# Kernel optimization log

Hardware: AMD Instinct MI355X
Metric: run time of the kernel (lower is better)

## Reference

```python
import jax, jax.numpy as jnp
import numpy as np

W_DIM, B_DIM, S = 8, 8, 900  # patches: [W, B, 1, 30, 30] -> seq_len 900


def setup_inputs() -> dict:
    key = jax.random.key(0)
    ks = jax.random.split(key, 8)
    radar = jax.random.normal(ks[0], (W_DIM, B_DIM, 1, 30, 30), jnp.float32)
    dmde = jax.random.normal(ks[1], (W_DIM, B_DIM, 1, 30, 30), jnp.float32)
    gumbel_u = jax.random.uniform(ks[2], (B_DIM * W_DIM, S, S), jnp.float32)
    # MHA with embed_dim=1 -> all projections are scalars (xavier-ish init)
    Wq = jax.random.normal(ks[3], (), jnp.float32)
    Wk = jax.random.normal(ks[4], (), jnp.float32)
    Wv = jax.random.normal(ks[5], (), jnp.float32)
    Wo = jax.random.normal(ks[6], (), jnp.float32)
    bq = jnp.zeros((), jnp.float32)
    bk = jnp.zeros((), jnp.float32)
    bv = jnp.zeros((), jnp.float32)
    bo = jnp.zeros((), jnp.float32)
    ln_gamma = jnp.ones((), jnp.float32)
    ln_beta = jnp.zeros((), jnp.float32)
    attn_residual_scale = jnp.asarray(1e-9, jnp.float32)
    return dict(radar_patches=radar, dmde_out_patches=dmde, gumbel_u=gumbel_u,
                Wq=Wq, bq=bq, Wk=Wk, bk=bk, Wv=Wv, bv=bv, Wo=Wo, bo=bo,
                ln_gamma=ln_gamma, ln_beta=ln_beta,
                attn_residual_scale=attn_residual_scale)


def reference(radar_patches, dmde_out_patches, gumbel_u, Wq, bq, Wk, bk, Wv, bv,
              Wo, bo, ln_gamma, ln_beta, attn_residual_scale):
    Wd, B = radar_patches.shape[0], radar_patches.shape[1]
    # [W,B,1,30,30] -> [B*W, S]
    radar = jnp.transpose(radar_patches, (1, 0, 2, 3, 4)).reshape(B * Wd, -1)
    mde = jnp.transpose(dmde_out_patches, (1, 0, 2, 3, 4)).reshape(B * Wd, -1)
    # --- cross attention, embed_dim = head_dim = 1 (scale = 1/sqrt(1) = 1) ---
    q = radar * Wq + bq
    k = mde * Wk + bk
    v = mde * Wv + bv
    attn = jax.nn.softmax(jnp.einsum('ni,nj->nij', q, k), axis=-1)  # [N,S,S]
    attended = jnp.einsum('nij,nj->ni', attn, v) * Wo + bo           # [N,S]
    # LayerNorm over last dim of size 1 (degenerate: output == ln_beta)
    x = (radar + attended)[..., None]                                # [N,S,1]
    mu = jnp.mean(x, axis=-1, keepdims=True)
    var = jnp.mean((x - mu) ** 2, axis=-1, keepdims=True)
    attended_out = (x - mu) / jnp.sqrt(var + 1e-5) * ln_gamma + ln_beta
    # --- hard gumbel attention gather/scatter, fully mask-vectorized ---
    valid = (radar != 0).astype(radar.dtype)                          # [N,S]
    noise = -jnp.log(-jnp.log(gumbel_u + 1e-8) + 1e-8)
    p = jax.nn.softmax(attn + noise, axis=-1)  # temperature = 1.0
    idx = jnp.argmax(p, axis=-1)                                      # [N,S]
    y_hard = jax.nn.one_hot(idx, p.shape[-1], dtype=p.dtype)
    y = jax.lax.stop_gradient(y_hard - p) + p                         # straight-through
    src = radar * valid   # invalid rows contribute nothing (matches per-row loop)
    out_seq = jnp.einsum('nts,nt->ns', y, src)[..., None]             # [N,S,1]
    combined = valid[..., None] * (out_seq != 0).astype(out_seq.dtype)
    out_seq = out_seq + combined * (attn_residual_scale * attended_out)
    # [N,S] -> [B,W,S] -> [B,1,S,W]
    out = out_seq[..., 0].reshape(B, Wd, -1).transpose(0, 2, 1)[:, None]
    return out
```

## Files before the change

### kernel.cpp

```cpp
#include <hip/hip_runtime.h>
#include <cfloat>

#define SS 900
#define WD 8
#define BD 8
#define NROWS 64
#define OUT_ELEMS (BD * SS * WD)
#define NQ 225
#define ROWS_PER_BLK 16
#define BLKS_PER_N 57
#define CAP 128

__global__ __launch_bounds__(256) void rel_zero(float4* __restrict__ out4) {
    int i = blockIdx.x * 256 + threadIdx.x;
    if (i < OUT_ELEMS / 4) out4[i] = make_float4(0.f, 0.f, 0.f, 0.f);
}

__global__ __launch_bounds__(256) void rel_main(
    const float* __restrict__ radar,
    const float* __restrict__ mde,
    const float* __restrict__ gumbel,
    const float* __restrict__ pWq, const float* __restrict__ pbq,
    const float* __restrict__ pWk, const float* __restrict__ pbk,
    float* __restrict__ out)
{
    const int tid   = threadIdx.x;
    const int n     = blockIdx.x / BLKS_PER_N;
    const int tbase = (blockIdx.x - n * BLKS_PER_N) * ROWS_PER_BLK;
    const int b     = n >> 3;
    const int w     = n & 7;

    __shared__ float4 ks4[NQ + 1];
    __shared__ float  s_red[8];
    __shared__ float  s_q[ROWS_PER_BLK], s_m[ROWS_PER_BLK], s_D[ROWS_PER_BLK];
    __shared__ unsigned long long s_win[ROWS_PER_BLK];
    __shared__ int    s_cnt;
    __shared__ int    s_qs[CAP];
    __shared__ float  s_qu[CAP];

    if (tid == 0) s_cnt = 0;
    if (tid < ROWS_PER_BLK) s_win[tid] = 0ULL;

    const float wk = pWk[0], bk0 = pbk[0];
    float kmin = FLT_MAX, kmax = -FLT_MAX;
    if (tid < NQ) {
        const float4* __restrict__ m4p = (const float4*)(mde + (size_t)(w * BD + b) * SS);
        float4 mq = m4p[tid];
        float4 k;
        k.x = __fmaf_rn(mq.x, wk, bk0);
        k.y = __fmaf_rn(mq.y, wk, bk0);
        k.z = __fmaf_rn(mq.z, wk, bk0);
        k.w = __fmaf_rn(mq.w, wk, bk0);
        ks4[tid] = k;
        kmin = fminf(fminf(k.x, k.y), fminf(k.z, k.w));
        kmax = fmaxf(fmaxf(k.x, k.y), fmaxf(k.z, k.w));
    }
    #pragma unroll
    for (int off = 1; off < 64; off <<= 1) {
        kmin = fminf(kmin, __shfl_xor(kmin, off, 64));
        kmax = fmaxf(kmax, __shfl_xor(kmax, off, 64));
    }
    if ((tid & 63) == 0) { s_red[tid >> 6] = kmin; s_red[4 + (tid >> 6)] = kmax; }
    __syncthreads();
    kmin = fminf(fminf(s_red[0], s_red[1]), fminf(s_red[2], s_red[3]));
    kmax = fmaxf(fmaxf(s_red[4], s_red[5]), fmaxf(s_red[6], s_red[7]));

    const int gg     = tid >> 4;
    const int lane16 = tid & 15;
    const int t      = tbase + gg;
    const bool active = (t < SS);
    const int tc     = active ? t : 0;
    const int row    = n * SS + tc;

    const float r0 = radar[(size_t)(w * BD + b) * SS + tc];
    const float q  = __fmaf_rn(r0, pWq[0], pbq[0]);
    const float m  = __fmul_rn(q, (q >= 0.0f) ? kmax : kmin);

    const float4* __restrict__ g4 = (const float4*)(gumbel + (size_t)row * SS);
    const float*  __restrict__ kf = (const float*)ks4;

    float M[15];
    float D = 0.0f;
    #pragma unroll
    for (int j = 0; j < 15; j++) {
        const int f = j * 16 + lane16;
        const bool valid = (j < 14) || (lane16 == 0);
        const int fc = valid ? f : 0;
        float4 u = g4[fc];
        float4 k = ks4[fc];
        if (!valid) { u.x = u.y = u.z = u.w = -1.0f; }
        M[j] = fmaxf(fmaxf(u.x, u.y), fmaxf(u.z, u.w));
        if (valid) {
            D += __expf(__fmaf_rn(q, k.x, -m)) + __expf(__fmaf_rn(q, k.y, -m))
               + __expf(__fmaf_rn(q, k.z, -m)) + __expf(__fmaf_rn(q, k.w, -m));
        }
    }
    float umax = M[0];
    #pragma unroll
    for (int j = 1; j < 15; j++) umax = fmaxf(umax, M[j]);
    #pragma unroll
    for (int off = 1; off < 16; off <<= 1) {
        umax = fmaxf(umax, __shfl_xor(umax, off, 16));
        D += __shfl_xor(D, off, 16);
    }
    if (active && lane16 == 0) { s_q[gg] = q; s_m[gg] = m; s_D[gg] = D; }

    float margin = __fmaf_rn(1.002f, 1.0f / D, 1e-6f);
    float w0    = -__logf(umax + 1e-8f);
    float nzmax = -__logf(w0 + 1e-8f);
    float T     = nzmax - margin;
    float wT    = __expf(-T);
    float uthr  = __expf(-(wT - 1e-8f)) - 1e-8f;
    uthr = uthr - fabsf(uthr) * 1e-5f - 1e-9f;

    if (active) {
        #pragma unroll
        for (int j = 0; j < 15; j++) {
            if (M[j] >= uthr) {
                const int f = j * 16 + lane16;
                const bool valid = (j < 14) || (lane16 == 0);
                const int fc = valid ? f : 0;
                float4 u = g4[fc];
                if (!valid) { u.x = u.y = u.z = u.w = -1.0f; }
                const int s0 = fc * 4;
                if (u.x >= uthr) { int i2 = atomicAdd(&s_cnt, 1); if (i2 < CAP) { s_qs[i2] = (gg << 10) | s0;       s_qu[i2] = u.x; } }
                if (u.y >= uthr) { int i2 = atomicAdd(&s_cnt, 1); if (i2 < CAP) { s_qs[i2] = (gg << 10) | (s0 + 1); s_qu[i2] = u.y; } }
                if (u.z >= uthr) { int i2 = atomicAdd(&s_cnt, 1); if (i2 < CAP) { s_qs[i2] = (gg << 10) | (s0 + 2); s_qu[i2] = u.z; } }
                if (u.w >= uthr) { int i2 = atomicAdd(&s_cnt, 1); if (i2 < CAP) { s_qs[i2] = (gg << 10) | (s0 + 3); s_qu[i2] = u.w; } }
            }
        }
    }
    __syncthreads();

    const int nc = min(s_cnt, CAP);
    if (tid < nc) {
        int   pk = s_qs[tid];
        int   g2 = pk >> 10, s = pk & 0x3FF;
        float u  = s_qu[tid];
        float q2 = s_q[g2], m2 = s_m[g2], D2 = s_D[g2];
        float l  = __fmul_rn(q2, kf[s]);
        float nz = -logf(-logf(u + 1e-8f) + 1e-8f);
        float v  = expf(l - m2) / D2 + nz;
        unsigned vb = __float_as_uint(v);
        unsigned key32 = (vb & 0x80000000u) ? ~vb : (vb | 0x80000000u);
        unsigned long long key =
            ((unsigned long long)key32 << 32) | (unsigned)(0xFFFFFFFFu - (unsigned)s);
        atomicMax(&s_win[g2], key);
    }
    __syncthreads();

    if (active && lane16 == 0) {
        unsigned long long key = s_win[gg];
        unsigned s = 0xFFFFFFFFu - (unsigned)(key & 0xFFFFFFFFull);
        atomicAdd(&out[((size_t)b * SS + s) * WD + w], r0);
    }
}

__global__ __launch_bounds__(256) void rel_epilogue(
    const float* __restrict__ radar,
    const float* __restrict__ pScale,
    const float* __restrict__ pBeta,
    float* __restrict__ out)
{
    int i = blockIdx.x * 256 + threadIdx.x;
    if (i >= OUT_ELEMS) return;
    int w    = i & 7;
    int rest = i >> 3;
    int s    = rest % SS;
    int b    = rest / SS;
    float o = out[i];
    float r = radar[(size_t)(w * BD + b) * SS + s];
    float add = ((r != 0.0f) && (o != 0.0f)) ? (pScale[0] * pBeta[0]) : 0.0f;
    out[i] = o + add;
}

extern "C" void kernel_launch(void* const* d_in, const int* in_sizes, int n_in,
                              void* d_out, int out_size, void* d_ws, size_t ws_size,
                              hipStream_t stream) {
    const float* radar  = (const float*)d_in[0];
    const float* mde    = (const float*)d_in[1];
    const float* gumbel = (const float*)d_in[2];
    const float* Wq     = (const float*)d_in[3];
    const float* bq     = (const float*)d_in[4];
    const float* Wk     = (const float*)d_in[5];
    const float* bk     = (const float*)d_in[6];
    const float* beta   = (const float*)d_in[12];
    const float* scale  = (const float*)d_in[13];
    float* out = (float*)d_out;

    rel_zero<<<(OUT_ELEMS / 4 + 255) / 256, 256, 0, stream>>>((float4*)out);
    rel_main<<<NROWS * BLKS_PER_N, 256, 0, stream>>>(radar, mde, gumbel,
                                                     Wq, bq, Wk, bk, out);
    rel_epilogue<<<(OUT_ELEMS + 255) / 256, 256, 0, stream>>>(radar, scale, beta, out);
}
```

Before: 44.55 us.

## Replace global atomic scatter with index buffer and shared-memory scatter kernel

The main kernel now writes each row's argmax index to a workspace buffer instead of doing a global atomicAdd into the output. A new per-sequence kernel accumulates radar values into shared memory with shared atomics and applies the epilogue residual in the same pass. This removes the separate zero-fill and epilogue launches and the global atomics, at the cost of a small extra index buffer round trip and only 64 blocks in the final kernel.

```diff
diff --git a/kernel.cpp b/kernel.cpp
--- a/kernel.cpp
+++ b/kernel.cpp
@@ -11,18 +11,13 @@
 #define BLKS_PER_N 57
 #define CAP 128
 
-__global__ __launch_bounds__(256) void rel_zero(float4* __restrict__ out4) {
-    int i = blockIdx.x * 256 + threadIdx.x;
-    if (i < OUT_ELEMS / 4) out4[i] = make_float4(0.f, 0.f, 0.f, 0.f);
-}
-
 __global__ __launch_bounds__(256) void rel_main(
     const float* __restrict__ radar,
     const float* __restrict__ mde,
     const float* __restrict__ gumbel,
     const float* __restrict__ pWq, const float* __restrict__ pbq,
     const float* __restrict__ pWk, const float* __restrict__ pbk,
-    float* __restrict__ out)
+    int* __restrict__ idxbuf)
 {
     const int tid   = threadIdx.x;
     const int n     = blockIdx.x / BLKS_PER_N;
@@ -152,26 +147,41 @@
     if (active && lane16 == 0) {
         unsigned long long key = s_win[gg];
         unsigned s = 0xFFFFFFFFu - (unsigned)(key & 0xFFFFFFFFull);
-        atomicAdd(&out[((size_t)b * SS + s) * WD + w], r0);
+        idxbuf[n * SS + t] = (int)s;
     }
 }
 
-__global__ __launch_bounds__(256) void rel_epilogue(
+__global__ __launch_bounds__(1024) void rel_final(
     const float* __restrict__ radar,
+    const int* __restrict__ idxbuf,
     const float* __restrict__ pScale,
     const float* __restrict__ pBeta,
     float* __restrict__ out)
 {
-    int i = blockIdx.x * 256 + threadIdx.x;
-    if (i >= OUT_ELEMS) return;
-    int w    = i & 7;
-    int rest = i >> 3;
-    int s    = rest % SS;
-    int b    = rest / SS;
-    float o = out[i];
-    float r = radar[(size_t)(w * BD + b) * SS + s];
-    float add = ((r != 0.0f) && (o != 0.0f)) ? (pScale[0] * pBeta[0]) : 0.0f;
-    out[i] = o + add;
+    const int n = blockIdx.x;
+    const int b = n >> 3, w = n & 7;
+    const int tid = threadIdx.x;
+
+    __shared__ float acc[SS];
+    __shared__ float rad[SS];
+
+    if (tid < SS) {
+        acc[tid] = 0.0f;
+        rad[tid] = radar[(size_t)(w * BD + b) * SS + tid];
+    }
+    __syncthreads();
+    if (tid < SS) {
+        int s = idxbuf[n * SS + tid];
+        atomicAdd(&acc[s], rad[tid]);
+    }
+    __syncthreads();
+    if (tid < SS) {
+        const float c = pScale[0] * pBeta[0];
+        float o = acc[tid];
+        float r = rad[tid];
+        out[((size_t)b * SS + tid) * WD + w] =
+            o + (((r != 0.0f) && (o != 0.0f)) ? c : 0.0f);
+    }
 }
 
 extern "C" void kernel_launch(void* const* d_in, const int* in_sizes, int n_in,
@@ -188,8 +198,9 @@
     const float* scale  = (const float*)d_in[13];
     float* out = (float*)d_out;
 
-    rel_zero<<<(OUT_ELEMS / 4 + 255) / 256, 256, 0, stream>>>((float4*)out);
+    int* idxbuf = (int*)d_ws;
+
     rel_main<<<NROWS * BLKS_PER_N, 256, 0, stream>>>(radar, mde, gumbel,
-                                                     Wq, bq, Wk, bk, out);
-    rel_epilogue<<<(OUT_ELEMS + 255) / 256, 256, 0, stream>>>(radar, scale, beta, out);
+                                                     Wq, bq, Wk, bk, idxbuf);
+    rel_final<<<NROWS, 1024, 0, stream>>>(radar, idxbuf, scale, beta, out);
 }
```

Result: faster. 41.16 us (median of 2 runs) (-7.6%).
